# Performance work log

Hardware: AMD Instinct MI355X
Metric: run time of the kernel (lower is better)

The kernel has to match this reference:

```python
import jax, jax.numpy as jnp
import numpy as np

OUT_H, OUT_W = 256, 256  # output_size from init_kwargs


def setup_inputs() -> dict:
    key = jax.random.key(0)
    k1, k2 = jax.random.split(key)
    x = jax.random.normal(k1, (32, 256, 256, 32), dtype=jnp.float32)
    theta = jax.random.normal(k2, (32, 6), dtype=jnp.float32)
    return {"x": x, "theta": theta}


def reference(x, theta):
    B, H, W, C = x.shape
    # regular grid in [-1,1], homogeneous coords: [3, OUT_H*OUT_W]
    xs = jnp.linspace(-1.0, 1.0, OUT_W)
    ys = jnp.linspace(-1.0, 1.0, OUT_H)
    gx, gy = jnp.meshgrid(xs, ys)  # [OUT_H, OUT_W]
    grid = jnp.stack([gx.ravel(), gy.ravel(), jnp.ones(OUT_H * OUT_W, jnp.float32)], axis=0)
    T = theta.reshape(B, 2, 3)
    sampled = jnp.einsum('bij,jp->bip', T, grid)  # [B, 2, P]
    sx = 0.5 * (sampled[:, 0, :] + 1.0) * W  # [B, P]
    sy = 0.5 * (sampled[:, 1, :] + 1.0) * H
    x0 = sx.astype(jnp.int32)  # truncation toward zero, matching tf cast
    y0 = sy.astype(jnp.int32)
    x1 = x0 + 1
    y1 = y0 + 1
    x0c = jnp.clip(x0, 0, W - 1)
    x1c = jnp.clip(x1, 0, W - 1)
    y0c = jnp.clip(y0, 0, H - 1)
    y1c = jnp.clip(y1, 0, H - 1)
    base = (jnp.arange(B, dtype=jnp.int32) * (H * W))[:, None]  # [B,1]
    flat = x.reshape(-1, C)  # [B*H*W, C]
    idx_a = base + y0c * W + x0c
    idx_b = base + y1c * W + x0c
    idx_c = base + y0c * W + x1c
    idx_d = base + y1c * W + x1c
    pa = jnp.take(flat, idx_a, axis=0)  # [B, P, C]
    pb = jnp.take(flat, idx_b, axis=0)
    pc = jnp.take(flat, idx_c, axis=0)
    pd = jnp.take(flat, idx_d, axis=0)
    x0f = x0c.astype(jnp.float32)
    x1f = x1c.astype(jnp.float32)
    y0f = y0c.astype(jnp.float32)
    y1f = y1c.astype(jnp.float32)
    wa = ((x1f - sx) * (y1f - sy))[..., None]
    wb = ((x1f - sx) * (sy - y0f))[..., None]
    wc = ((sx - x0f) * (y1f - sy))[..., None]
    wd = ((sx - x0f) * (sy - y0f))[..., None]
    out = wa * pa + wb * pb + wc * pc + wd * pd  # [B, P, C]
    return out.reshape(B, OUT_H, OUT_W, C)
```

## Files before the change

### kernel.cpp

```cpp
#include <hip/hip_runtime.h>


#define B_  32
#define H_  256
#define W_  256
#define C_  32
#define P_  (H_ * W_)

__global__ __launch_bounds__(256) void stn_kernel(
    const float* __restrict__ x,
    const float* __restrict__ theta,
    float* __restrict__ out)
{
    __shared__ double t[6];

    const long long gid = (long long)blockIdx.x * 256 + threadIdx.x;
    const int p   = (int)(gid >> 3);
    const int v   = (int)(gid & 7);
    const int b   = p >> 16;
    const int rem = p & 65535;
    const int py  = rem >> 8;
    const int px  = rem & 255;

    if (threadIdx.x < 6) t[threadIdx.x] = (double)theta[b * 6 + threadIdx.x];
    __syncthreads();

    const double gx = (2.0 * (double)px) / 255.0 - 1.0;
    const double gy = (2.0 * (double)py) / 255.0 - 1.0;

    const double sxs = t[0] * gx + t[1] * gy + t[2];
    const double sys = t[3] * gx + t[4] * gy + t[5];

    const double sx = 0.5 * (sxs + 1.0) * (double)W_;
    const double sy = 0.5 * (sys + 1.0) * (double)H_;

    const int x0 = (int)sx;
    const int y0 = (int)sy;
    const int x1 = x0 + 1;
    const int y1 = y0 + 1;

    const int x0c = min(max(x0, 0), W_ - 1);
    const int x1c = min(max(x1, 0), W_ - 1);
    const int y0c = min(max(y0, 0), H_ - 1);
    const int y1c = min(max(y1, 0), H_ - 1);

    const double x0f = (double)x0c, x1f = (double)x1c;
    const double y0f = (double)y0c, y1f = (double)y1c;

    const float wa = (float)((x1f - sx) * (y1f - sy));
    const float wb = (float)((x1f - sx) * (sy - y0f));
    const float wc = (float)((sx - x0f) * (y1f - sy));
    const float wd = (float)((sx - x0f) * (sy - y0f));

    const long long base = (long long)b * (H_ * W_);
    const long long ia = (base + (long long)(y0c * W_ + x0c)) * C_ + v * 4;
    const long long ib = (base + (long long)(y1c * W_ + x0c)) * C_ + v * 4;
    const long long ic = (base + (long long)(y0c * W_ + x1c)) * C_ + v * 4;
    const long long id = (base + (long long)(y1c * W_ + x1c)) * C_ + v * 4;

    const float4 pa = *reinterpret_cast<const float4*>(x + ia);
    const float4 pb = *reinterpret_cast<const float4*>(x + ib);
    const float4 pc = *reinterpret_cast<const float4*>(x + ic);
    const float4 pd = *reinterpret_cast<const float4*>(x + id);

    float4 r;
    r.x = wa * pa.x + wb * pb.x + wc * pc.x + wd * pd.x;
    r.y = wa * pa.y + wb * pb.y + wc * pc.y + wd * pd.y;
    r.z = wa * pa.z + wb * pb.z + wc * pc.z + wd * pd.z;
    r.w = wa * pa.w + wb * pb.w + wc * pc.w + wd * pd.w;

    *reinterpret_cast<float4*>(out + (long long)p * C_ + v * 4) = r;
}

extern "C" void kernel_launch(void* const* d_in, const int* in_sizes, int n_in,
                              void* d_out, int out_size, void* d_ws, size_t ws_size,
                              hipStream_t stream) {
    const float* x     = (const float*)d_in[0];
    const float* theta = (const float*)d_in[1];
    float* out         = (float*)d_out;

    const int total_threads = B_ * P_ * 8;
    const int block = 256;
    const int grid = total_threads / block;

    stn_kernel<<<grid, block, 0, stream>>>(x, theta, out);
}
```

Before: 420.0 us.

## Tile output into 8x4 pixel blocks and use nontemporal stores

```diff
diff --git a/kernel.cpp b/kernel.cpp
--- a/kernel.cpp
+++ b/kernel.cpp
@@ -5,7 +5,11 @@
 #define H_  256
 #define W_  256
 #define C_  32
-#define P_  (H_ * W_)
+
+#define TX_ 8
+#define TY_ 4
+
+typedef float floatx4 __attribute__((ext_vector_type(4)));
 
 __global__ __launch_bounds__(256) void stn_kernel(
     const float* __restrict__ x,
@@ -14,15 +18,17 @@
 {
     __shared__ double t[6];
 
-    const long long gid = (long long)blockIdx.x * 256 + threadIdx.x;
-    const int p   = (int)(gid >> 3);
-    const int v   = (int)(gid & 7);
-    const int b   = p >> 16;
-    const int rem = p & 65535;
-    const int py  = rem >> 8;
-    const int px  = rem & 255;
+    const int tid = threadIdx.x;
+    const int v   = tid & 7;
+    const int pxl = tid >> 3;
+    const int tx  = pxl & (TX_ - 1);
+    const int ty  = pxl >> 3;
 
-    if (threadIdx.x < 6) t[threadIdx.x] = (double)theta[b * 6 + threadIdx.x];
+    const int px = blockIdx.x * TX_ + tx;
+    const int py = blockIdx.y * TY_ + ty;
+    const int b  = blockIdx.z;
+
+    if (tid < 6) t[tid] = (double)theta[b * 6 + tid];
     __syncthreads();
 
     const double gx = (2.0 * (double)px) / 255.0 - 1.0;
@@ -58,18 +64,16 @@
     const long long ic = (base + (long long)(y0c * W_ + x1c)) * C_ + v * 4;
     const long long id = (base + (long long)(y1c * W_ + x1c)) * C_ + v * 4;
 
-    const float4 pa = *reinterpret_cast<const float4*>(x + ia);
-    const float4 pb = *reinterpret_cast<const float4*>(x + ib);
-    const float4 pc = *reinterpret_cast<const float4*>(x + ic);
-    const float4 pd = *reinterpret_cast<const float4*>(x + id);
+    const floatx4 pa = *reinterpret_cast<const floatx4*>(x + ia);
+    const floatx4 pb = *reinterpret_cast<const floatx4*>(x + ib);
+    const floatx4 pc = *reinterpret_cast<const floatx4*>(x + ic);
+    const floatx4 pd = *reinterpret_cast<const floatx4*>(x + id);
 
-    float4 r;
-    r.x = wa * pa.x + wb * pb.x + wc * pc.x + wd * pd.x;
-    r.y = wa * pa.y + wb * pb.y + wc * pc.y + wd * pd.y;
-    r.z = wa * pa.z + wb * pb.z + wc * pc.z + wd * pd.z;
-    r.w = wa * pa.w + wb * pb.w + wc * pc.w + wd * pd.w;
+    floatx4 r = wa * pa + wb * pb + wc * pc + wd * pd;
 
-    *reinterpret_cast<float4*>(out + (long long)p * C_ + v * 4) = r;
+    const long long po = (long long)((b << 16) | (py << 8) | px);
+    __builtin_nontemporal_store(r,
+        reinterpret_cast<floatx4*>(out + po * C_ + v * 4));
 }
 
 extern "C" void kernel_launch(void* const* d_in, const int* in_sizes, int n_in,
@@ -79,9 +83,8 @@
     const float* theta = (const float*)d_in[1];
     float* out         = (float*)d_out;
 
-    const int total_threads = B_ * P_ * 8;
-    const int block = 256;
-    const int grid = total_threads / block;
+    dim3 grid(W_ / TX_, H_ / TY_, B_);
+    dim3 block(256);
 
     stn_kernel<<<grid, block, 0, stream>>>(x, theta, out);
 }
```

Result: no change. 413.8 us (-1.5%).
